# Performance work log

Measured on AMD Instinct MI355X. Metric: run time of the kernel, lower is better.

The kernel has to match this reference:

```python
import jax, jax.numpy as jnp
import numpy as np

MARGIN = 0.3
EPS = 1e-6  # torch pairwise_distance default eps used by TripletMarginLoss


def setup_inputs() -> dict:
    key = jax.random.key(0)
    k1, k2 = jax.random.split(key)
    emb = jax.random.normal(k1, (4096, 256), dtype=jnp.float32)
    emb = emb / jnp.linalg.norm(emb, axis=1, keepdims=True)  # docstring: normalized embeddings
    labels = jax.random.randint(k2, (4096,), 0, 64, dtype=jnp.int64) if jax.config.jax_enable_x64 else jax.random.randint(k2, (4096,), 0, 64, dtype=jnp.int32)
    return {"embeddings": emb, "labels": labels}


def _triplet_mining_loss(embeddings, labels):
    B = embeddings.shape[0]
    # pairwise euclidean distances via GEMM (matches torch.cdist p=2)
    sq = jnp.sum(embeddings * embeddings, axis=1)
    d2 = sq[:, None] + sq[None, :] - 2.0 * (embeddings @ embeddings.T)
    dist = jnp.sqrt(jnp.maximum(d2, 0.0))  # [B, B]

    same = labels[:, None] == labels[None, :]
    eye = jnp.eye(B, dtype=bool)
    pos_mask = same & ~eye
    neg_mask = ~same
    valid = pos_mask.any(axis=1) & neg_mask.any(axis=1)

    # hardest positive per anchor
    ap = jnp.where(pos_mask, dist, -jnp.inf)
    hp_idx = jnp.argmax(ap, axis=1)                           # [B]
    ap_dist = jnp.take_along_axis(dist, hp_idx[:, None], 1)[:, 0]

    # semi-hard negative: ap < d_an < ap + margin; pick FIRST such index (original takes semi_hard_indices[0])
    semi = neg_mask & (dist > ap_dist[:, None]) & (dist < ap_dist[:, None] + MARGIN)
    any_semi = semi.any(axis=1)
    first_semi = jnp.argmax(semi, axis=1)                     # argmax of bool = first True
    an = jnp.where(neg_mask, dist, jnp.inf)
    hardest_neg = jnp.argmin(an, axis=1)
    neg_idx = jnp.where(any_semi, first_semi, hardest_neg)

    # triplet margin loss recomputed from embeddings (torch adds EPS inside the norm)
    pos_e = embeddings[hp_idx]
    neg_e = embeddings[neg_idx]
    d_ap = jnp.linalg.norm(embeddings - pos_e + EPS, axis=1)
    d_an = jnp.linalg.norm(embeddings - neg_e + EPS, axis=1)
    per_anchor = jnp.maximum(d_ap - d_an + MARGIN, 0.0)

    vf = valid.astype(embeddings.dtype)
    cnt = jnp.sum(vf)
    return jnp.where(cnt > 0, jnp.sum(per_anchor * vf) / jnp.maximum(cnt, 1.0), 0.0)


def reference(embeddings, labels):
    return _triplet_mining_loss(embeddings, labels)
```

## Files before the change

### kernel.cpp

```cpp
#include <hip/hip_runtime.h>
#include <math.h>

#define BN 4096
#define DIM 256
#define D4 (DIM/4)
#define MI 8
#define MARGINF 0.3f
#define EPSF 1e-6f
#define SCAP 96
#define IMAX 0x7fffffff
#define PCAP 128

typedef __attribute__((ext_vector_type(8))) short bf16x8;
typedef __attribute__((ext_vector_type(4))) float f32x4;

__device__ __forceinline__ float fma4(float4 a, float4 b, float c){
  return fmaf(a.x,b.x, fmaf(a.y,b.y, fmaf(a.z,b.z, fmaf(a.w,b.w, c))));
}
__device__ __forceinline__ unsigned short f2bf(float x){
  unsigned u = __float_as_uint(x);
  return (unsigned short)((u + 0x7FFFu + ((u>>16)&1u)) >> 16);
}
__device__ __forceinline__ float bf2f(unsigned short h){
  return __uint_as_float(((unsigned)h)<<16);
}

__global__ __launch_bounds__(256) void k_pre2(const float* __restrict__ E,
     const int* __restrict__ labels,
     unsigned short* __restrict__ EhiT, unsigned short* __restrict__ EloT,
     float* __restrict__ sq, unsigned int* __restrict__ counter,
     unsigned short* __restrict__ memb, int* __restrict__ cntC,
     unsigned long long* __restrict__ negKey, unsigned int* __restrict__ semiJ){
  int t = threadIdx.x, l = t&63, w = t>>6;
  int g = blockIdx.x;
  const float4* E4 = (const float4*)E;
  bf16x8* HT = (bf16x8*)EhiT;
  bf16x8* LT = (bf16x8*)EloT;
  #pragma unroll
  for (int it=0; it<2; it++){
    int idx = it*256 + t;
    int kk = idx>>6, sub = idx&63, q = sub>>4, n = sub&15;
    int r = g*16 + n;
    int c = kk*4 + q;
    float4 v0 = E4[(size_t)r*64 + c*2];
    float4 v1 = E4[(size_t)r*64 + c*2 + 1];
    unsigned short h[8], lo[8];
    float vv[8] = {v0.x,v0.y,v0.z,v0.w, v1.x,v1.y,v1.z,v1.w};
    #pragma unroll
    for (int i=0;i<8;i++){ h[i]=f2bf(vv[i]); lo[i]=f2bf(vv[i]-bf2f(h[i])); }
    bf16x8 hv, lv;
    #pragma unroll
    for (int i=0;i<8;i++){ hv[i]=(short)h[i]; lv[i]=(short)lo[i]; }
    size_t d = (size_t)g*512 + idx;
    HT[d] = hv; LT[d] = lv;
  }
  int row = t>>4, part = t&15;
  const float4* rp = E4 + (size_t)(g*16+row)*64 + part*4;
  float s0 = fma4(rp[0],rp[0],0.f);
  float s1 = fma4(rp[1],rp[1],0.f);
  s0 = fma4(rp[2],rp[2],s0);
  s1 = fma4(rp[3],rp[3],s1);
  float s = s0+s1;
  s += __shfl_xor(s,1); s += __shfl_xor(s,2); s += __shfl_xor(s,4); s += __shfl_xor(s,8);
  if (part==0) sq[g*16+row] = s;
  if (g==0 && t==0) counter[0] = 0u;

  if (g < 16){
    int c = g*4 + w;
    int cnt = 0;
    for (int ch=0; ch<64; ch++){
      int j = ch*64 + l;
      bool m = (labels[j] == c);
      unsigned long long mask = __ballot(m);
      if (m){
        int pos = cnt + __popcll(mask & ((1ull<<l)-1ull));
        if (pos < PCAP-4) memb[c*PCAP + pos] = (unsigned short)j;
      }
      cnt += __popcll(mask);
    }
    if (cnt > PCAP-4) cnt = PCAP-4;
    if (l < 4) memb[c*PCAP + cnt + l] = 0;
    if (l == 0) cntC[c] = cnt;
  } else if (g < 32){
    int i = (g-16)*256 + t;
    negKey[i] = ~0ull;
    semiJ[i]  = 0xFFFFFFFFu;
  }
}

__global__ __launch_bounds__(256) void k_posm(const float* __restrict__ E,
     const int* __restrict__ labels, const float* __restrict__ sq,
     const unsigned short* __restrict__ memb, const int* __restrict__ cntC,
     float* __restrict__ apw, int* __restrict__ hpw){
  int t=threadIdx.x, l=t&63, w=t>>6;
  int aw = blockIdx.x*4 + w;
  int c = labels[aw];
  float sqa = sq[aw];
  const float4* E4 = (const float4*)E;
  float4 areg = E4[(size_t)aw*64 + l];
  int cnt = cntC[c];
  const unsigned short* lst = memb + c*PCAP;
  float bv2 = -INFINITY; int bj = IMAX;
  #pragma unroll 2
  for (int base=0; base<cnt; base+=4){
    int j0 = lst[base+0], j1 = lst[base+1], j2 = lst[base+2], j3 = lst[base+3];
    float4 r0v = E4[(size_t)j0*64 + l];
    float4 r1v = E4[(size_t)j1*64 + l];
    float4 r2v = E4[(size_t)j2*64 + l];
    float4 r3v = E4[(size_t)j3*64 + l];
    float p0 = fma4(areg, r0v, 0.f);
    float p1 = fma4(areg, r1v, 0.f);
    float p2 = fma4(areg, r2v, 0.f);
    float p3 = fma4(areg, r3v, 0.f);
    #pragma unroll
    for (int off=32; off; off>>=1){
      p0 += __shfl_xor(p0, off); p1 += __shfl_xor(p1, off);
      p2 += __shfl_xor(p2, off); p3 += __shfl_xor(p3, off);
    }
    float d0 = sqa + sq[j0] - 2.0f*p0;
    float d1 = sqa + sq[j1] - 2.0f*p1;
    float d2 = sqa + sq[j2] - 2.0f*p2;
    float d3 = sqa + sq[j3] - 2.0f*p3;
    if (j0 != aw && (d0 > bv2 || (d0 == bv2 && j0 < bj))){ bv2=d0; bj=j0; }
    if (base+1 < cnt && j1 != aw && (d1 > bv2 || (d1 == bv2 && j1 < bj))){ bv2=d1; bj=j1; }
    if (base+2 < cnt && j2 != aw && (d2 > bv2 || (d2 == bv2 && j2 < bj))){ bv2=d2; bj=j2; }
    if (base+3 < cnt && j3 != aw && (d3 > bv2 || (d3 == bv2 && j3 < bj))){ bv2=d3; bj=j3; }
  }
  if (l==0){
    apw[aw] = (bj==IMAX) ? -INFINITY : sqrtf(fmaxf(bv2, 0.0f));
    hpw[aw] = (bj==IMAX) ? 0 : bj;
  }
}

__global__ __launch_bounds__(1024,4) void k_negm(
     const unsigned short* __restrict__ EhiT, const unsigned short* __restrict__ EloT,
     const int* __restrict__ labels, const float* __restrict__ sq,
     const float* __restrict__ apw,
     unsigned long long* __restrict__ negKey, unsigned int* __restrict__ semiJ){
  __shared__ bf16x8 afH[1024];
  __shared__ bf16x8 afL[1024];
  __shared__ __align__(16) int   labsH[1024];
  __shared__ __align__(16) float sqH[1024];
  __shared__ float rnv[16][32]; __shared__ int rnj[16][32]; __shared__ int rsm[16][32];
  int t=threadIdx.x, l=t&63, w=t>>6;
  int lane16 = l&15, quad = l>>4;
  int q8    = blockIdx.x & 7;
  int split = q8 >> 1;
  int grp   = (blockIdx.x >> 3)*2 + (q8 & 1);
  int a0 = grp*32;
  int hbase = split*1024;
  const bf16x8* HT = (const bf16x8*)EhiT;
  const bf16x8* LT = (const bf16x8*)EloT;
  afH[t] = HT[(size_t)grp*1024 + t];
  afL[t] = LT[(size_t)grp*1024 + t];
  labsH[t] = labels[hbase + t];
  sqH[t]   = sq[hbase + t];
  float sqa[2][4]; int laba[2][4]; float ap2[2][4]; float th2[2][4];
  #pragma unroll
  for (int g=0; g<2; g++){
    #pragma unroll
    for (int r=0; r<4; r++){
      int ag = a0 + g*16 + quad*4 + r;
      sqa[g][r] = sq[ag]; laba[g][r] = labels[ag];
      float ap = apw[ag];
      ap2[g][r] = ap*ap;
      float th = ap + MARGINF;
      th2[g][r] = th*th;
    }
  }
  __syncthreads();
  float mn[2][4]; int mj[2][4]; int sm[2][4];
  #pragma unroll
  for (int g=0; g<2; g++)
    #pragma unroll
    for (int r=0; r<4; r++){ mn[g][r]=INFINITY; mj[g][r]=IMAX; sm[g][r]=IMAX; }
  #pragma unroll 1
  for (int tile=0; tile<4; tile++){
    int gl = w*4 + tile;
    size_t BBase = (size_t)(split*64 + gl) * 512;
    f32x4 acc00={0.f,0.f,0.f,0.f}, acc01=acc00, acc02=acc00;
    f32x4 acc10=acc00, acc11=acc00, acc12=acc00;
    #pragma unroll 2
    for (int kk=0; kk<8; kk++){
      bf16x8 bh  = HT[BBase + kk*64 + l];
      bf16x8 bl  = LT[BBase + kk*64 + l];
      bf16x8 ah0 = afH[kk*64 + l];
      bf16x8 al0 = afL[kk*64 + l];
      bf16x8 ah1 = afH[512 + kk*64 + l];
      bf16x8 al1 = afL[512 + kk*64 + l];
      acc00 = __builtin_amdgcn_mfma_f32_16x16x32_bf16(ah0, bh, acc00, 0,0,0);
      acc01 = __builtin_amdgcn_mfma_f32_16x16x32_bf16(ah0, bl, acc01, 0,0,0);
      acc02 = __builtin_amdgcn_mfma_f32_16x16x32_bf16(al0, bh, acc02, 0,0,0);
      acc10 = __builtin_amdgcn_mfma_f32_16x16x32_bf16(ah1, bh, acc10, 0,0,0);
      acc11 = __builtin_amdgcn_mfma_f32_16x16x32_bf16(ah1, bl, acc11, 0,0,0);
      acc12 = __builtin_amdgcn_mfma_f32_16x16x32_bf16(al1, bh, acc12, 0,0,0);
    }
    int jloc = gl*16 + lane16;
    int lj = labsH[jloc]; float sqj = sqH[jloc];
    int jglob = hbase + jloc;
    #pragma unroll
    for (int r=0; r<4; r++){
      float dot0 = acc00[r] + (acc01[r] + acc02[r]);
      float d20  = sqa[0][r] + sqj - 2.0f*dot0;
      if (lj != laba[0][r]){
        if (d20 < mn[0][r]){ mn[0][r]=d20; mj[0][r]=jglob; }
        if (d20 > ap2[0][r] && d20 < th2[0][r] && jglob < sm[0][r]) sm[0][r]=jglob;
      }
      float dot1 = acc10[r] + (acc11[r] + acc12[r]);
      float d21  = sqa[1][r] + sqj - 2.0f*dot1;
      if (lj != laba[1][r]){
        if (d21 < mn[1][r]){ mn[1][r]=d21; mj[1][r]=jglob; }
        if (d21 > ap2[1][r] && d21 < th2[1][r] && jglob < sm[1][r]) sm[1][r]=jglob;
      }
    }
  }
  #pragma unroll
  for (int g=0; g<2; g++){
    #pragma unroll
    for (int r=0; r<4; r++){
      float v=mn[g][r]; int j=mj[g][r]; int s=sm[g][r];
      #pragma unroll
      for (int off=1; off<16; off<<=1){
        float v2=__shfl_xor(v,off); int j2=__shfl_xor(j,off); int s2=__shfl_xor(s,off);
        if (v2<v || (v2==v && j2<j)){ v=v2; j=j2; }
        s = (s2<s)?s2:s;
      }
      if (lane16==0){
        int ai = g*16 + quad*4 + r;
        rnv[w][ai]=v; rnj[w][ai]=j; rsm[w][ai]=s;
      }
    }
  }
  __syncthreads();
  if (t < 32){
    float V=INFINITY; int J=IMAX; int S=IMAX;
    for (int q=0; q<16; q++){
      float v2=rnv[q][t]; int j2=rnj[q][t];
      if (v2<V || (v2==V && j2<J)){ V=v2; J=j2; }
      int s2=rsm[q][t]; S=(s2<S)?s2:S;
    }
    unsigned u = __float_as_uint(V);
    unsigned key = (u & 0x80000000u) ? ~u : (u | 0x80000000u);
    unsigned long long k64 = (((unsigned long long)key)<<32) | (unsigned)J;
    atomicMin(&negKey[a0+t], k64);
    if (S != IMAX) atomicMin(&semiJ[a0+t], (unsigned)S);
  }
}

__global__ __launch_bounds__(256) void k_fin2(const float* __restrict__ E,
     const float* __restrict__ apw, const int* __restrict__ hpw,
     const unsigned long long* __restrict__ negKey, const unsigned int* __restrict__ semiJ,
     float* __restrict__ partials, unsigned int* __restrict__ counter,
     float* __restrict__ out){
  __shared__ float lsumS[4], lcntS[4];
  __shared__ float rs[4], rc[4];
  __shared__ int lastFlag;
  int t=threadIdx.x, l=t&63, w=t>>6;
  const float4* E4 = (const float4*)E;
  float lsum=0.f, lcnt=0.f;
  #pragma unroll 1
  for (int i=0;i<4;i++){
    int a = blockIdx.x*16 + w*4 + i;
    unsigned long long k64 = negKey[a];
    unsigned Jn = (unsigned)(k64 & 0xFFFFFFFFull);
    unsigned Sn = semiJ[a];
    bool anyneg = (Jn != (unsigned)IMAX);
    int ng = (Sn != 0xFFFFFFFFu) ? (int)Sn : (int)Jn;
    float ap = apw[a];
    bool dov = (ap != -INFINITY) && anyneg;
    if (dov){
      int hp = hpw[a];
      float4 av = E4[(size_t)a*64 + l];
      float4 pv = E4[(size_t)hp*64 + l];
      float4 nv = E4[(size_t)ng*64 + l];
      float d0=av.x-pv.x+EPSF, d1=av.y-pv.y+EPSF, d2=av.z-pv.z+EPSF, d3=av.w-pv.w+EPSF;
      float sp = fmaf(d0,d0, fmaf(d1,d1, fmaf(d2,d2, d3*d3)));
      float n0=av.x-nv.x+EPSF, n1=av.y-nv.y+EPSF, n2=av.z-nv.z+EPSF, n3=av.w-nv.w+EPSF;
      float sn = fmaf(n0,n0, fmaf(n1,n1, fmaf(n2,n2, n3*n3)));
      #pragma unroll
      for (int off=32; off; off>>=1){ sp += __shfl_xor(sp,off); sn += __shfl_xor(sn,off); }
      lsum += fmaxf(sqrtf(sp)-sqrtf(sn)+MARGINF, 0.0f);
      lcnt += 1.0f;
    }
  }
  if (l==0){ lsumS[w]=lsum; lcntS[w]=lcnt; }
  __syncthreads();
  if (t==0){
    partials[2*blockIdx.x]   = (lsumS[0]+lsumS[1])+(lsumS[2]+lsumS[3]);
    partials[2*blockIdx.x+1] = (lcntS[0]+lcntS[1])+(lcntS[2]+lcntS[3]);
    __threadfence();
    unsigned int old = atomicAdd(counter, 1u);
    lastFlag = (old == gridDim.x - 1) ? 1 : 0;
  }
  __syncthreads();
  if (lastFlag){
    __threadfence();
    float s = partials[2*t], c = partials[2*t+1];
    #pragma unroll
    for (int off=32; off; off>>=1){ s += __shfl_xor(s,off); c += __shfl_xor(c,off); }
    if (l==0){ rs[w]=s; rc[w]=c; }
    __syncthreads();
    if (t==0){
      float S=(rs[0]+rs[1])+(rs[2]+rs[3]);
      float C=(rc[0]+rc[1])+(rc[2]+rc[3]);
      out[0] = (C>0.0f) ? S/fmaxf(C,1.0f) : 0.0f;
    }
  }
}

__global__ __launch_bounds__(256) void k_sq(const float* __restrict__ E, float* __restrict__ sq){
  int i = blockIdx.x*256 + threadIdx.x;
  if (i >= BN) return;
  const float4* r = (const float4*)E + (size_t)i*D4;
  float a0=0.f,a1=0.f,a2=0.f,a3=0.f;
  #pragma unroll
  for (int q=0;q<D4;q+=4){
    a0 = fma4(r[q],r[q],a0);   a1 = fma4(r[q+1],r[q+1],a1);
    a2 = fma4(r[q+2],r[q+2],a2); a3 = fma4(r[q+3],r[q+3],a3);
  }
  sq[i] = (a0+a1)+(a2+a3);
}

__global__ __launch_bounds__(256) void k_pos(const float* __restrict__ E, const int* __restrict__ labels,
                       const float* __restrict__ sq, float* __restrict__ apw,
                       int* __restrict__ hpw, int* __restrict__ anypw){
  __shared__ int members[1024];
  __shared__ float4 mem4[SCAP*65];
  __shared__ int cnts[16][4];
  __shared__ int offs[16][4];
  __shared__ int cntS;
  int t = threadIdx.x, lane = t&63, w = t>>6;
  int c = blockIdx.x >> 2, split = blockIdx.x & 3;
  for (int ch=0; ch<16; ch++){
    bool m = (labels[ch*256 + t] == c);
    unsigned long long mask = __ballot(m);
    if (lane==0) cnts[ch][w] = __popcll(mask);
  }
  __syncthreads();
  if (t==0){
    int run=0;
    for (int ch=0; ch<16; ch++)
      for (int q=0;q<4;q++){ offs[ch][q]=run; run+=cnts[ch][q]; }
    cntS = run;
  }
  __syncthreads();
  int cnt = cntS; if (cnt>1024) cnt=1024;
  for (int ch=0; ch<16; ch++){
    int idx = ch*256 + t;
    bool m = (labels[idx] == c);
    unsigned long long mask = __ballot(m);
    int my = __popcll(mask & ((1ull<<lane)-1ull));
    int pos = offs[ch][w] + my;
    if (m && pos < 1024) members[pos] = idx;
  }
  int S = (cnt < SCAP) ? cnt : SCAP;
  int anyp = (cnt >= 2) ? 1 : 0;
  __syncthreads();
  const float4* E4 = (const float4*)E;
  for (int idx=t; idx<S*64; idx+=256){
    int row = idx>>6, f = idx&63;
    mem4[row*65 + f] = E4[(size_t)members[row]*D4 + f];
  }
  __syncthreads();
  int esplit = split*4 + w;
  int p = lane&3, cand = lane>>2;
  int passes = (cnt+15)>>4;
  for (int mi=esplit; mi<cnt; mi+=16){
    int i = members[mi];
    float sqi = sq[i];
    float4 ai4[16];
    if (mi < S){
      #pragma unroll
      for (int m=0;m<16;m++) ai4[m] = mem4[mi*65 + p + 4*m];
    } else {
      #pragma unroll
      for (int m=0;m<16;m++) ai4[m] = E4[(size_t)i*D4 + p + 4*m];
    }
    float bv = -INFINITY; int bj = IMAX;
    for (int ps=0; ps<passes; ps++){
      int mj = ps*16 + cand;
      if (mj < cnt && mj != mi){
        int j = members[mj];
        float a0v=0.f, a1v=0.f;
        if (mj < S){
          const float4* rj = mem4 + mj*65 + p;
          #pragma unroll
          for (int m=0;m<16;m+=2){ a0v=fma4(ai4[m],rj[4*m],a0v); a1v=fma4(ai4[m+1],rj[4*(m+1)],a1v); }
        } else {
          const float4* rj = E4 + (size_t)j*D4 + p;
          #pragma unroll
          for (int m=0;m<16;m+=2){ a0v=fma4(ai4[m],rj[4*m],a0v); a1v=fma4(ai4[m+1],rj[4*(m+1)],a1v); }
        }
        float acc = a0v+a1v;
        acc += __shfl_xor(acc,1); acc += __shfl_xor(acc,2);
        float d = sqrtf(fmaxf(sqi + sq[j] - 2.0f*acc, 0.0f));
        if (p==0){ if (d > bv || (d==bv && j<bj)){ bv=d; bj=j; } }
      }
    }
    #pragma unroll
    for (int off=32; off; off>>=1){
      float v2=__shfl_xor(bv,off); int j2=__shfl_xor(bj,off);
      if (v2>bv || (v2==bv && j2<bj)){ bv=v2; bj=j2; }
    }
    if (lane==0){
      int J = (bj==IMAX) ? 0 : bj;
      apw[i]=bv; hpw[i]=J; anypw[i]=anyp;
    }
  }
}

__global__ __launch_bounds__(256,2) void k_main(const float* __restrict__ E, const int* __restrict__ labels,
     const float* __restrict__ sq, const float* __restrict__ apw, const int* __restrict__ hpw,
     const int* __restrict__ anypw, float* __restrict__ partials){
  __shared__ float4 At[MI*68 + 4];
  __shared__ float redv[4][MI]; __shared__ int redj[4][MI]; __shared__ int redsm[4][MI];
  __shared__ int finNeg[MI]; __shared__ int finVal[MI];
  __shared__ float redp[4], redn[4];
  int t=threadIdx.x, lane=t&63, w=t>>6;
  int a0 = blockIdx.x * MI;
  const float4* E4 = (const float4*)E;
  for (int idx=t; idx<MI*64; idx+=256){
    int a=idx>>6, q=idx&63, pp=q&3, mm=q>>2;
    At[a*68 + pp*17 + mm] = E4[(size_t)(a0+a)*D4 + q];
  }
  __syncthreads();
  float apv[MI], sqi[MI]; int labi[MI];
  #pragma unroll
  for (int a=0;a<MI;a++){ apv[a]=apw[a0+a]; sqi[a]=sq[a0+a]; labi[a]=labels[a0+a]; }
  float mnv[MI]; int mnj[MI]; int smj[MI];
  #pragma unroll
  for (int a=0;a<MI;a++){ mnv[a]=INFINITY; mnj[a]=0; smj[a]=IMAX; }
  int s = t>>2, p = t&3;
  for (int it=0; it<16; it++){
    int colb = it*256 + 4*s;
    const float4* __restrict__ bp = E4 + (size_t)colb*D4 + p;
    float acc[MI][4];
    #pragma unroll
    for (int a=0;a<MI;a++){
      #pragma unroll
      for (int c2=0;c2<4;c2++) acc[a][c2]=0.0f;
    }
    for (int mg=0; mg<4; mg++){
      float4 b[4][4];
      #pragma unroll
      for (int c2=0;c2<4;c2++){
        #pragma unroll
        for (int m=0;m<4;m++) b[m][c2] = bp[(size_t)c2*D4 + mg*16 + m*4];
      }
      #pragma unroll
      for (int a=0;a<MI;a++){
        float4 a4[4];
        #pragma unroll
        for (int m=0;m<4;m++) a4[m] = At[a*68 + p*17 + mg*4 + m];
        #pragma unroll
        for (int m=0;m<4;m++){
          #pragma unroll
          for (int c2=0;c2<4;c2++) acc[a][c2] = fma4(a4[m], b[m][c2], acc[a][c2]);
        }
      }
    }
    #pragma unroll
    for (int a=0;a<MI;a++){
      #pragma unroll
      for (int c2=0;c2<4;c2++){
        float v = acc[a][c2];
        v += __shfl_xor(v,1); v += __shfl_xor(v,2);
        acc[a][c2] = v;
      }
    }
    #pragma unroll
    for (int c2=0;c2<4;c2++){
      int j = colb + c2;
      int lj = labels[j]; float sqj = sq[j];
      #pragma unroll
      for (int a=0;a<MI;a++){
        float d = sqrtf(fmaxf(sqi[a]+sqj-2.0f*acc[a][c2], 0.0f));
        if (lj != labi[a]){
          if (d < mnv[a]){ mnv[a]=d; mnj[a]=j; }
          if (d > apv[a] && d < apv[a]+MARGINF && j < smj[a]) smj[a]=j;
        }
      }
    }
  }
  #pragma unroll
  for (int a=0;a<MI;a++){
    float v=mnv[a]; int j=mnj[a]; int sm=smj[a];
    #pragma unroll
    for (int off=32; off; off>>=1){
      float v2=__shfl_xor(v,off); int j2=__shfl_xor(j,off); int s2=__shfl_xor(sm,off);
      if (v2<v || (v2==v && j2<j)){ v=v2; j=j2; }
      sm = (s2<sm)?s2:sm;
    }
    if (lane==0){ redv[w][a]=v; redj[w][a]=j; redsm[w][a]=sm; }
  }
  __syncthreads();
  if (t < MI){
    int a=t;
    float V=INFINITY; int J=0; int S=IMAX; bool first=true;
    for (int q=0;q<4;q++){
      float v2=redv[q][a]; int j2=redj[q][a];
      if (first || v2<V || (v2==V && j2<J)){ V=v2; J=j2; first=false; }
      int s2=redsm[q][a]; S=(s2<S)?s2:S;
    }
    bool anyneg = (V < INFINITY);
    finNeg[a] = (S != IMAX) ? S : J;
    finVal[a] = (anypw[a0+a] != 0 && anyneg) ? 1 : 0;
  }
  __syncthreads();
  float lsum=0.0f, lcnt=0.0f;
  for (int a=0;a<MI;a++){
    if (finVal[a]){
      int hp = hpw[a0+a]; int ng = finNeg[a];
      float ai = E[(size_t)(a0+a)*DIM + t];
      float pv = E[(size_t)hp*DIM + t];
      float nv = E[(size_t)ng*DIM + t];
      float dp = ai - pv + EPSF; float dn = ai - nv + EPSF;
      float sp = dp*dp, sn = dn*dn;
      #pragma unroll
      for (int off=32; off; off>>=1){ sp += __shfl_xor(sp,off); sn += __shfl_xor(sn,off); }
      if (lane==0){ redp[w]=sp; redn[w]=sn; }
    }
    __syncthreads();
    if (finVal[a] && t==0){
      float SP=(redp[0]+redp[1])+(redp[2]+redp[3]);
      float SN=(redn[0]+redn[1])+(redn[2]+redn[3]);
      lsum += fmaxf(sqrtf(SP)-sqrtf(SN)+MARGINF, 0.0f);
      lcnt += 1.0f;
    }
    __syncthreads();
  }
  if (t==0){ partials[2*blockIdx.x]=lsum; partials[2*blockIdx.x+1]=lcnt; }
}

__global__ __launch_bounds__(256) void k_fin(const float* __restrict__ partials, float* __restrict__ out, int nb){
  __shared__ float rs[4], rc[4];
  int t=threadIdx.x, lane=t&63, w=t>>6;
  float s=0.f, c=0.f;
  for (int q=t;q<nb;q+=256){ s+=partials[2*q]; c+=partials[2*q+1]; }
  #pragma unroll
  for (int off=32; off; off>>=1){ s+=__shfl_xor(s,off); c+=__shfl_xor(c,off); }
  if (lane==0){ rs[w]=s; rc[w]=c; }
  __syncthreads();
  if (t==0){
    float S=(rs[0]+rs[1])+(rs[2]+rs[3]);
    float C=(rc[0]+rc[1])+(rc[2]+rc[3]);
    out[0] = (C>0.0f) ? S/fmaxf(C,1.0f) : 0.0f;
  }
}

extern "C" void kernel_launch(void* const* d_in, const int* in_sizes, int n_in,
                              void* d_out, int out_size, void* d_ws, size_t ws_size,
                              hipStream_t stream) {
  const float* E      = (const float*)d_in[0];
  const int*   labels = (const int*)d_in[1];
  float* out = (float*)d_out;

  float* sqw      = (float*)d_ws;
  float* apw      = sqw + BN;
  int*   hpw      = (int*)(apw + BN);
  int*   anypw    = hpw + BN;
  float* partials = (float*)(anypw + BN);
  unsigned int* counter = (unsigned int*)(partials + 1024);
  unsigned long long* negKey = (unsigned long long*)((char*)d_ws + 72*1024);
  unsigned int*       semiJ  = (unsigned int*)((char*)d_ws + 104*1024);
  unsigned short* memb = (unsigned short*)((char*)d_ws + 48*1024);
  int* cntC = (int*)((char*)d_ws + 120*1024);
  unsigned short* EhiT = (unsigned short*)((char*)d_ws + 131072);
  unsigned short* EloT = EhiT + (size_t)BN*DIM;
  bool big = ws_size >= (size_t)(131072 + 4*1024*1024);

  if (big){
    k_pre2<<<256,  256,  0, stream>>>(E, labels, EhiT, EloT, sqw, counter, memb, cntC, negKey, semiJ);
    k_posm<<<1024, 256,  0, stream>>>(E, labels, sqw, memb, cntC, apw, hpw);
    k_negm<<<512,  1024, 0, stream>>>(EhiT, EloT, labels, sqw, apw, negKey, semiJ);
    k_fin2<<<256,  256,  0, stream>>>(E, apw, hpw, negKey, semiJ, partials, counter, out);
  } else {
    k_sq  <<<BN/256, 256, 0, stream>>>(E, sqw);
    k_pos <<<256,    256, 0, stream>>>(E, labels, sqw, apw, hpw, anypw);
    k_main<<<BN/MI,  256, 0, stream>>>(E, labels, sqw, apw, hpw, anypw, partials);
    k_fin <<<1,      256, 0, stream>>>(partials, out, BN/MI);
  }
}
```

Baseline: 162.8 us.

## Fuse positive mining, negative mining and final loss into one kernel

Merges the hardest-positive kernel, the MFMA negative-mining kernel and the final loss kernel into one fused kernel. Each block now computes its own anchors' positives, then mines negatives over half of the candidates (2048 instead of 1024, with a 256-block grid). The last of the two blocks per anchor group finishes that group's loss and accumulates it through fixed-point 64-bit atomics, and a global done counter triggers the final division. The preprocessing kernel stages rows in LDS, parallelises the label-membership scan across waves and software-prefetches the B fragments. This cuts two launches and the global round trips, at the cost of halving the grid, which may lower occupancy and add serial positive-mining work per block.

```diff
diff --git a/kernel.cpp b/kernel.cpp
--- a/kernel.cpp
+++ b/kernel.cpp
@@ -10,6 +10,7 @@
 #define SCAP 96
 #define IMAX 0x7fffffff
 #define PCAP 128
+#define FXSCALE 1099511627776.0f
 
 typedef __attribute__((ext_vector_type(8))) short bf16x8;
 typedef __attribute__((ext_vector_type(4))) float f32x4;
@@ -25,176 +26,228 @@
   return __uint_as_float(((unsigned)h)<<16);
 }
 
-__global__ __launch_bounds__(256) void k_pre2(const float* __restrict__ E,
+__global__ __launch_bounds__(256) void k_pre(const float* __restrict__ E,
      const int* __restrict__ labels,
      unsigned short* __restrict__ EhiT, unsigned short* __restrict__ EloT,
-     float* __restrict__ sq, unsigned int* __restrict__ counter,
+     float* __restrict__ sq,
      unsigned short* __restrict__ memb, int* __restrict__ cntC,
-     unsigned long long* __restrict__ negKey, unsigned int* __restrict__ semiJ){
+     unsigned long long* __restrict__ negKey, unsigned int* __restrict__ semiJ,
+     int* __restrict__ cntA, unsigned long long* __restrict__ gsum,
+     unsigned long long* __restrict__ gcnt, unsigned int* __restrict__ done){
+  __shared__ float4 eS[16*65];
+  __shared__ unsigned long long msk[4][16];
+  __shared__ int wcnt[4];
   int t = threadIdx.x, l = t&63, w = t>>6;
   int g = blockIdx.x;
   const float4* E4 = (const float4*)E;
+  #pragma unroll
+  for (int it=0; it<4; it++){
+    int idx = it*256 + t;
+    int row = idx>>6, f = idx&63;
+    eS[row*65 + f] = E4[(size_t)g*1024 + idx];
+  }
+  __syncthreads();
   bf16x8* HT = (bf16x8*)EhiT;
   bf16x8* LT = (bf16x8*)EloT;
   #pragma unroll
   for (int it=0; it<2; it++){
-    int idx = it*256 + t;
-    int kk = idx>>6, sub = idx&63, q = sub>>4, n = sub&15;
-    int r = g*16 + n;
-    int c = kk*4 + q;
-    float4 v0 = E4[(size_t)r*64 + c*2];
-    float4 v1 = E4[(size_t)r*64 + c*2 + 1];
-    unsigned short h[8], lo[8];
+    int u = it*256 + t;
+    int kk = u>>6, sub = u&63, q = sub>>4, n = sub&15;
+    float4 v0 = eS[n*65 + kk*8 + q*2];
+    float4 v1 = eS[n*65 + kk*8 + q*2 + 1];
     float vv[8] = {v0.x,v0.y,v0.z,v0.w, v1.x,v1.y,v1.z,v1.w};
-    #pragma unroll
-    for (int i=0;i<8;i++){ h[i]=f2bf(vv[i]); lo[i]=f2bf(vv[i]-bf2f(h[i])); }
     bf16x8 hv, lv;
     #pragma unroll
-    for (int i=0;i<8;i++){ hv[i]=(short)h[i]; lv[i]=(short)lo[i]; }
-    size_t d = (size_t)g*512 + idx;
-    HT[d] = hv; LT[d] = lv;
-  }
-  int row = t>>4, part = t&15;
-  const float4* rp = E4 + (size_t)(g*16+row)*64 + part*4;
-  float s0 = fma4(rp[0],rp[0],0.f);
-  float s1 = fma4(rp[1],rp[1],0.f);
-  s0 = fma4(rp[2],rp[2],s0);
-  s1 = fma4(rp[3],rp[3],s1);
-  float s = s0+s1;
-  s += __shfl_xor(s,1); s += __shfl_xor(s,2); s += __shfl_xor(s,4); s += __shfl_xor(s,8);
-  if (part==0) sq[g*16+row] = s;
-  if (g==0 && t==0) counter[0] = 0u;
-
-  if (g < 16){
-    int c = g*4 + w;
-    int cnt = 0;
-    for (int ch=0; ch<64; ch++){
-      int j = ch*64 + l;
-      bool m = (labels[j] == c);
+    for (int i=0;i<8;i++){
+      unsigned short h = f2bf(vv[i]);
+      unsigned short lo = f2bf(vv[i]-bf2f(h));
+      hv[i]=(short)h; lv[i]=(short)lo;
+    }
+    HT[(size_t)g*512 + u] = hv;
+    LT[(size_t)g*512 + u] = lv;
+  }
+  {
+    int row = t>>4, part = t&15;
+    const float4* rp = &eS[row*65 + part*4];
+    float s0 = fma4(rp[0],rp[0],0.f);
+    float s1 = fma4(rp[1],rp[1],0.f);
+    s0 = fma4(rp[2],rp[2],s0);
+    s1 = fma4(rp[3],rp[3],s1);
+    float s = s0+s1;
+    s += __shfl_xor(s,1); s += __shfl_xor(s,2); s += __shfl_xor(s,4); s += __shfl_xor(s,8);
+    if (part==0) sq[g*16+row] = s;
+  }
+
+  if (g < 64){
+    int c = g;
+    int local = 0;
+    for (int i=0;i<16;i++){
+      int ch = w*16 + i;
+      bool m = (labels[ch*64 + l] == c);
       unsigned long long mask = __ballot(m);
+      if (l==0) msk[w][i] = mask;
+      local += __popcll(mask);
+    }
+    if (l==0) wcnt[w] = local;
+    __syncthreads();
+    int off = 0;
+    #pragma unroll
+    for (int q2=0; q2<4; q2++) if (q2 < w) off += wcnt[q2];
+    int total = wcnt[0]+wcnt[1]+wcnt[2]+wcnt[3];
+    int run = off;
+    for (int i=0;i<16;i++){
+      unsigned long long mask = msk[w][i];
+      int ch = w*16 + i;
+      bool m = (mask >> l) & 1ull;
       if (m){
-        int pos = cnt + __popcll(mask & ((1ull<<l)-1ull));
-        if (pos < PCAP-4) memb[c*PCAP + pos] = (unsigned short)j;
-      }
-      cnt += __popcll(mask);
-    }
-    if (cnt > PCAP-4) cnt = PCAP-4;
-    if (l < 4) memb[c*PCAP + cnt + l] = 0;
-    if (l == 0) cntC[c] = cnt;
-  } else if (g < 32){
-    int i = (g-16)*256 + t;
+        int pos = run + __popcll(mask & ((1ull<<l)-1ull));
+        if (pos < PCAP-4) memb[c*PCAP + pos] = (unsigned short)(ch*64 + l);
+      }
+      run += __popcll(mask);
+    }
+    if (total > PCAP-4) total = PCAP-4;
+    if (t < 4) memb[c*PCAP + total + t] = 0;
+    if (t == 0) cntC[c] = total;
+  } else if (g < 80){
+    int i = (g-64)*256 + t;
     negKey[i] = ~0ull;
     semiJ[i]  = 0xFFFFFFFFu;
-  }
-}
-
-__global__ __launch_bounds__(256) void k_posm(const float* __restrict__ E,
+  } else if (g == 80){
+    if (t < 128) cntA[t] = 0;
+    if (t == 128) *gsum = 0ull;
+    if (t == 129) *gcnt = 0ull;
+    if (t == 130) *done = 0u;
+  }
+}
+
+__global__ __launch_bounds__(1024,4) void k_fused(const float* __restrict__ E,
+     const unsigned short* __restrict__ EhiT, const unsigned short* __restrict__ EloT,
      const int* __restrict__ labels, const float* __restrict__ sq,
      const unsigned short* __restrict__ memb, const int* __restrict__ cntC,
-     float* __restrict__ apw, int* __restrict__ hpw){
-  int t=threadIdx.x, l=t&63, w=t>>6;
-  int aw = blockIdx.x*4 + w;
-  int c = labels[aw];
-  float sqa = sq[aw];
-  const float4* E4 = (const float4*)E;
-  float4 areg = E4[(size_t)aw*64 + l];
-  int cnt = cntC[c];
-  const unsigned short* lst = memb + c*PCAP;
-  float bv2 = -INFINITY; int bj = IMAX;
-  #pragma unroll 2
-  for (int base=0; base<cnt; base+=4){
-    int j0 = lst[base+0], j1 = lst[base+1], j2 = lst[base+2], j3 = lst[base+3];
-    float4 r0v = E4[(size_t)j0*64 + l];
-    float4 r1v = E4[(size_t)j1*64 + l];
-    float4 r2v = E4[(size_t)j2*64 + l];
-    float4 r3v = E4[(size_t)j3*64 + l];
-    float p0 = fma4(areg, r0v, 0.f);
-    float p1 = fma4(areg, r1v, 0.f);
-    float p2 = fma4(areg, r2v, 0.f);
-    float p3 = fma4(areg, r3v, 0.f);
-    #pragma unroll
-    for (int off=32; off; off>>=1){
-      p0 += __shfl_xor(p0, off); p1 += __shfl_xor(p1, off);
-      p2 += __shfl_xor(p2, off); p3 += __shfl_xor(p3, off);
-    }
-    float d0 = sqa + sq[j0] - 2.0f*p0;
-    float d1 = sqa + sq[j1] - 2.0f*p1;
-    float d2 = sqa + sq[j2] - 2.0f*p2;
-    float d3 = sqa + sq[j3] - 2.0f*p3;
-    if (j0 != aw && (d0 > bv2 || (d0 == bv2 && j0 < bj))){ bv2=d0; bj=j0; }
-    if (base+1 < cnt && j1 != aw && (d1 > bv2 || (d1 == bv2 && j1 < bj))){ bv2=d1; bj=j1; }
-    if (base+2 < cnt && j2 != aw && (d2 > bv2 || (d2 == bv2 && j2 < bj))){ bv2=d2; bj=j2; }
-    if (base+3 < cnt && j3 != aw && (d3 > bv2 || (d3 == bv2 && j3 < bj))){ bv2=d3; bj=j3; }
-  }
-  if (l==0){
-    apw[aw] = (bj==IMAX) ? -INFINITY : sqrtf(fmaxf(bv2, 0.0f));
-    hpw[aw] = (bj==IMAX) ? 0 : bj;
-  }
-}
-
-__global__ __launch_bounds__(1024,4) void k_negm(
-     const unsigned short* __restrict__ EhiT, const unsigned short* __restrict__ EloT,
-     const int* __restrict__ labels, const float* __restrict__ sq,
-     const float* __restrict__ apw,
-     unsigned long long* __restrict__ negKey, unsigned int* __restrict__ semiJ){
+     unsigned long long* __restrict__ negKey, unsigned int* __restrict__ semiJ,
+     int* __restrict__ cntA, unsigned long long* __restrict__ gsum,
+     unsigned long long* __restrict__ gcnt, unsigned int* __restrict__ done,
+     float* __restrict__ out){
   __shared__ bf16x8 afH[1024];
   __shared__ bf16x8 afL[1024];
-  __shared__ __align__(16) int   labsH[1024];
-  __shared__ __align__(16) float sqH[1024];
+  __shared__ __align__(16) int   labsH[2048];
+  __shared__ __align__(16) float sqH[2048];
   __shared__ float rnv[16][32]; __shared__ int rnj[16][32]; __shared__ int rsm[16][32];
+  __shared__ float apS[32]; __shared__ int hpS[32]; __shared__ int okS[32];
+  __shared__ float ap2S[32]; __shared__ float th2S[32];
+  __shared__ unsigned long long lfx; __shared__ unsigned int lcn;
+  __shared__ int lastFlag;
   int t=threadIdx.x, l=t&63, w=t>>6;
   int lane16 = l&15, quad = l>>4;
-  int q8    = blockIdx.x & 7;
-  int split = q8 >> 1;
-  int grp   = (blockIdx.x >> 3)*2 + (q8 & 1);
+  int q8   = blockIdx.x & 7;
+  int half = q8 >> 2;
+  int grp  = (blockIdx.x >> 3)*4 + (q8 & 3);
   int a0 = grp*32;
-  int hbase = split*1024;
+  int hbase = half*2048;
   const bf16x8* HT = (const bf16x8*)EhiT;
   const bf16x8* LT = (const bf16x8*)EloT;
+  const float4* E4 = (const float4*)E;
   afH[t] = HT[(size_t)grp*1024 + t];
   afL[t] = LT[(size_t)grp*1024 + t];
-  labsH[t] = labels[hbase + t];
-  sqH[t]   = sq[hbase + t];
+  { int2   lv = ((const int2*)(labels + hbase))[t];
+    labsH[2*t] = lv.x; labsH[2*t+1] = lv.y;
+    float2 sv = ((const float2*)(sq + hbase))[t];
+    sqH[2*t] = sv.x; sqH[2*t+1] = sv.y; }
+  if (t==0){ lfx = 0ull; lcn = 0u; }
+
+  for (int s=0; s<2; s++){
+    int ai = 2*w + s;
+    int aw = a0 + ai;
+    int c = labels[aw];
+    float sqa_ = sq[aw];
+    float4 areg = E4[(size_t)aw*64 + l];
+    int cn = cntC[c];
+    const unsigned short* lst = memb + c*PCAP;
+    float bv2 = -INFINITY; int bj = IMAX;
+    #pragma unroll 2
+    for (int base=0; base<cn; base+=4){
+      int j0 = lst[base+0], j1 = lst[base+1], j2 = lst[base+2], j3 = lst[base+3];
+      float4 r0v = E4[(size_t)j0*64 + l];
+      float4 r1v = E4[(size_t)j1*64 + l];
+      float4 r2v = E4[(size_t)j2*64 + l];
+      float4 r3v = E4[(size_t)j3*64 + l];
+      float p0 = fma4(areg, r0v, 0.f);
+      float p1 = fma4(areg, r1v, 0.f);
+      float p2 = fma4(areg, r2v, 0.f);
+      float p3 = fma4(areg, r3v, 0.f);
+      #pragma unroll
+      for (int off=32; off; off>>=1){
+        p0 += __shfl_xor(p0, off); p1 += __shfl_xor(p1, off);
+        p2 += __shfl_xor(p2, off); p3 += __shfl_xor(p3, off);
+      }
+      float d0 = sqa_ + sq[j0] - 2.0f*p0;
+      float d1 = sqa_ + sq[j1] - 2.0f*p1;
+      float d2 = sqa_ + sq[j2] - 2.0f*p2;
+      float d3 = sqa_ + sq[j3] - 2.0f*p3;
+      if (j0 != aw && (d0 > bv2 || (d0 == bv2 && j0 < bj))){ bv2=d0; bj=j0; }
+      if (base+1 < cn && j1 != aw && (d1 > bv2 || (d1 == bv2 && j1 < bj))){ bv2=d1; bj=j1; }
+      if (base+2 < cn && j2 != aw && (d2 > bv2 || (d2 == bv2 && j2 < bj))){ bv2=d2; bj=j2; }
+      if (base+3 < cn && j3 != aw && (d3 > bv2 || (d3 == bv2 && j3 < bj))){ bv2=d3; bj=j3; }
+    }
+    if (l==0){
+      okS[ai] = (bj != IMAX);
+      apS[ai] = (bj==IMAX) ? -INFINITY : sqrtf(fmaxf(bv2, 0.0f));
+      hpS[ai] = (bj==IMAX) ? 0 : bj;
+    }
+  }
+  __syncthreads();
+  if (t < 32){
+    float ap = apS[t];
+    ap2S[t] = ap*ap;
+    float th = ap + MARGINF;
+    th2S[t] = th*th;
+  }
+  __syncthreads();
+
   float sqa[2][4]; int laba[2][4]; float ap2[2][4]; float th2[2][4];
   #pragma unroll
   for (int g=0; g<2; g++){
     #pragma unroll
     for (int r=0; r<4; r++){
-      int ag = a0 + g*16 + quad*4 + r;
+      int ai = g*16 + quad*4 + r;
+      int ag = a0 + ai;
       sqa[g][r] = sq[ag]; laba[g][r] = labels[ag];
-      float ap = apw[ag];
-      ap2[g][r] = ap*ap;
-      float th = ap + MARGINF;
-      th2[g][r] = th*th;
-    }
-  }
-  __syncthreads();
+      ap2[g][r] = ap2S[ai]; th2[g][r] = th2S[ai];
+    }
+  }
+
   float mn[2][4]; int mj[2][4]; int sm[2][4];
   #pragma unroll
   for (int g=0; g<2; g++)
     #pragma unroll
     for (int r=0; r<4; r++){ mn[g][r]=INFINITY; mj[g][r]=IMAX; sm[g][r]=IMAX; }
+#define STEPK(KK,BH,BL) { \
+    bf16x8 ah0=afH[(KK)*64+l], al0=afL[(KK)*64+l]; \
+    bf16x8 ah1=afH[512+(KK)*64+l], al1=afL[512+(KK)*64+l]; \
+    acc00=__builtin_amdgcn_mfma_f32_16x16x32_bf16(ah0,BH,acc00,0,0,0); \
+    acc01=__builtin_amdgcn_mfma_f32_16x16x32_bf16(ah0,BL,acc01,0,0,0); \
+    acc02=__builtin_amdgcn_mfma_f32_16x16x32_bf16(al0,BH,acc02,0,0,0); \
+    acc10=__builtin_amdgcn_mfma_f32_16x16x32_bf16(ah1,BH,acc10,0,0,0); \
+    acc11=__builtin_amdgcn_mfma_f32_16x16x32_bf16(ah1,BL,acc11,0,0,0); \
+    acc12=__builtin_amdgcn_mfma_f32_16x16x32_bf16(al1,BH,acc12,0,0,0); }
   #pragma unroll 1
-  for (int tile=0; tile<4; tile++){
-    int gl = w*4 + tile;
-    size_t BBase = (size_t)(split*64 + gl) * 512;
+  for (int tile=0; tile<8; tile++){
+    int gl = w*8 + tile;
+    size_t BBase = (size_t)(half*128 + gl) * 512;
     f32x4 acc00={0.f,0.f,0.f,0.f}, acc01=acc00, acc02=acc00;
     f32x4 acc10=acc00, acc11=acc00, acc12=acc00;
-    #pragma unroll 2
-    for (int kk=0; kk<8; kk++){
-      bf16x8 bh  = HT[BBase + kk*64 + l];
-      bf16x8 bl  = LT[BBase + kk*64 + l];
-      bf16x8 ah0 = afH[kk*64 + l];
-      bf16x8 al0 = afL[kk*64 + l];
-      bf16x8 ah1 = afH[512 + kk*64 + l];
-      bf16x8 al1 = afL[512 + kk*64 + l];
-      acc00 = __builtin_amdgcn_mfma_f32_16x16x32_bf16(ah0, bh, acc00, 0,0,0);
-      acc01 = __builtin_amdgcn_mfma_f32_16x16x32_bf16(ah0, bl, acc01, 0,0,0);
-      acc02 = __builtin_amdgcn_mfma_f32_16x16x32_bf16(al0, bh, acc02, 0,0,0);
-      acc10 = __builtin_amdgcn_mfma_f32_16x16x32_bf16(ah1, bh, acc10, 0,0,0);
-      acc11 = __builtin_amdgcn_mfma_f32_16x16x32_bf16(ah1, bl, acc11, 0,0,0);
-      acc12 = __builtin_amdgcn_mfma_f32_16x16x32_bf16(al1, bh, acc12, 0,0,0);
-    }
+    bf16x8 bh0 = HT[BBase + 0*64 + l], bl0 = LT[BBase + 0*64 + l];
+    bf16x8 bh1 = HT[BBase + 1*64 + l], bl1 = LT[BBase + 1*64 + l];
+    bf16x8 bh2 = HT[BBase + 2*64 + l], bl2 = LT[BBase + 2*64 + l];
+    bf16x8 bh3 = HT[BBase + 3*64 + l], bl3 = LT[BBase + 3*64 + l];
+    STEPK(0,bh0,bl0); bh0 = HT[BBase + 4*64 + l]; bl0 = LT[BBase + 4*64 + l];
+    STEPK(1,bh1,bl1); bh1 = HT[BBase + 5*64 + l]; bl1 = LT[BBase + 5*64 + l];
+    STEPK(2,bh2,bl2); bh2 = HT[BBase + 6*64 + l]; bl2 = LT[BBase + 6*64 + l];
+    STEPK(3,bh3,bl3); bh3 = HT[BBase + 7*64 + l]; bl3 = LT[BBase + 7*64 + l];
+    STEPK(4,bh0,bl0);
+    STEPK(5,bh1,bl1);
+    STEPK(6,bh2,bl2);
+    STEPK(7,bh3,bl3);
     int jloc = gl*16 + lane16;
     int lj = labsH[jloc]; float sqj = sqH[jloc];
     int jglob = hbase + jloc;
@@ -214,6 +267,7 @@
       }
     }
   }
+#undef STEPK
   #pragma unroll
   for (int g=0; g<2; g++){
     #pragma unroll
@@ -245,65 +299,57 @@
     atomicMin(&negKey[a0+t], k64);
     if (S != IMAX) atomicMin(&semiJ[a0+t], (unsigned)S);
   }
-}
-
-__global__ __launch_bounds__(256) void k_fin2(const float* __restrict__ E,
-     const float* __restrict__ apw, const int* __restrict__ hpw,
-     const unsigned long long* __restrict__ negKey, const unsigned int* __restrict__ semiJ,
-     float* __restrict__ partials, unsigned int* __restrict__ counter,
-     float* __restrict__ out){
-  __shared__ float lsumS[4], lcntS[4];
-  __shared__ float rs[4], rc[4];
-  __shared__ int lastFlag;
-  int t=threadIdx.x, l=t&63, w=t>>6;
-  const float4* E4 = (const float4*)E;
-  float lsum=0.f, lcnt=0.f;
-  #pragma unroll 1
-  for (int i=0;i<4;i++){
-    int a = blockIdx.x*16 + w*4 + i;
-    unsigned long long k64 = negKey[a];
-    unsigned Jn = (unsigned)(k64 & 0xFFFFFFFFull);
-    unsigned Sn = semiJ[a];
-    bool anyneg = (Jn != (unsigned)IMAX);
-    int ng = (Sn != 0xFFFFFFFFu) ? (int)Sn : (int)Jn;
-    float ap = apw[a];
-    bool dov = (ap != -INFINITY) && anyneg;
-    if (dov){
-      int hp = hpw[a];
-      float4 av = E4[(size_t)a*64 + l];
-      float4 pv = E4[(size_t)hp*64 + l];
-      float4 nv = E4[(size_t)ng*64 + l];
-      float d0=av.x-pv.x+EPSF, d1=av.y-pv.y+EPSF, d2=av.z-pv.z+EPSF, d3=av.w-pv.w+EPSF;
-      float sp = fmaf(d0,d0, fmaf(d1,d1, fmaf(d2,d2, d3*d3)));
-      float n0=av.x-nv.x+EPSF, n1=av.y-nv.y+EPSF, n2=av.z-nv.z+EPSF, n3=av.w-nv.w+EPSF;
-      float sn = fmaf(n0,n0, fmaf(n1,n1, fmaf(n2,n2, n3*n3)));
-      #pragma unroll
-      for (int off=32; off; off>>=1){ sp += __shfl_xor(sp,off); sn += __shfl_xor(sn,off); }
-      lsum += fmaxf(sqrtf(sp)-sqrtf(sn)+MARGINF, 0.0f);
-      lcnt += 1.0f;
-    }
-  }
-  if (l==0){ lsumS[w]=lsum; lcntS[w]=lcnt; }
   __syncthreads();
   if (t==0){
-    partials[2*blockIdx.x]   = (lsumS[0]+lsumS[1])+(lsumS[2]+lsumS[3]);
-    partials[2*blockIdx.x+1] = (lcntS[0]+lcntS[1])+(lcntS[2]+lcntS[3]);
     __threadfence();
-    unsigned int old = atomicAdd(counter, 1u);
-    lastFlag = (old == gridDim.x - 1) ? 1 : 0;
+    int old = atomicAdd(&cntA[grp], 1);
+    lastFlag = (old == 1) ? 1 : 0;
   }
   __syncthreads();
   if (lastFlag){
     __threadfence();
-    float s = partials[2*t], c = partials[2*t+1];
-    #pragma unroll
-    for (int off=32; off; off>>=1){ s += __shfl_xor(s,off); c += __shfl_xor(c,off); }
-    if (l==0){ rs[w]=s; rc[w]=c; }
+    for (int s=0; s<2; s++){
+      int ai = 2*w + s;
+      int a = a0 + ai;
+      unsigned long long k64 = negKey[a];
+      unsigned Jn = (unsigned)(k64 & 0xFFFFFFFFull);
+      unsigned Sn = semiJ[a];
+      bool anyneg = (k64 != ~0ull);
+      int ng = (Sn != 0xFFFFFFFFu) ? (int)Sn : (int)Jn;
+      bool dov = (okS[ai] != 0) && anyneg;
+      float sp = 0.f, sn_ = 0.f;
+      if (dov){
+        int hp = hpS[ai];
+        float4 av = E4[(size_t)a*64 + l];
+        float4 pv = E4[(size_t)hp*64 + l];
+        float4 nv = E4[(size_t)ng*64 + l];
+        float d0=av.x-pv.x+EPSF, d1=av.y-pv.y+EPSF, d2=av.z-pv.z+EPSF, d3=av.w-pv.w+EPSF;
+        sp = fmaf(d0,d0, fmaf(d1,d1, fmaf(d2,d2, d3*d3)));
+        float n0=av.x-nv.x+EPSF, n1=av.y-nv.y+EPSF, n2=av.z-nv.z+EPSF, n3=av.w-nv.w+EPSF;
+        sn_ = fmaf(n0,n0, fmaf(n1,n1, fmaf(n2,n2, n3*n3)));
+      }
+      #pragma unroll
+      for (int off=32; off; off>>=1){ sp += __shfl_xor(sp,off); sn_ += __shfl_xor(sn_,off); }
+      if (l==0 && dov){
+        float loss = fmaxf(sqrtf(sp)-sqrtf(sn_)+MARGINF, 0.0f);
+        unsigned long long fx = (unsigned long long)llrintf(loss * FXSCALE);
+        atomicAdd(&lfx, fx);
+        atomicAdd(&lcn, 1u);
+      }
+    }
     __syncthreads();
     if (t==0){
-      float S=(rs[0]+rs[1])+(rs[2]+rs[3]);
-      float C=(rc[0]+rc[1])+(rc[2]+rc[3]);
-      out[0] = (C>0.0f) ? S/fmaxf(C,1.0f) : 0.0f;
+      atomicAdd(gsum, lfx);
+      atomicAdd(gcnt, (unsigned long long)lcn);
+      __threadfence();
+      unsigned int d = atomicAdd(done, 1u);
+      if (d == 127u){
+        __threadfence();
+        unsigned long long S = atomicAdd(gsum, 0ull);
+        unsigned long long C = atomicAdd(gcnt, 0ull);
+        double Sf = (double)S / 1099511627776.0;
+        out[0] = (C > 0ull) ? (float)(Sf / (double)C) : 0.0f;
+      }
     }
   }
 }
@@ -560,20 +606,23 @@
   int*   hpw      = (int*)(apw + BN);
   int*   anypw    = hpw + BN;
   float* partials = (float*)(anypw + BN);
-  unsigned int* counter = (unsigned int*)(partials + 1024);
   unsigned long long* negKey = (unsigned long long*)((char*)d_ws + 72*1024);
   unsigned int*       semiJ  = (unsigned int*)((char*)d_ws + 104*1024);
   unsigned short* memb = (unsigned short*)((char*)d_ws + 48*1024);
   int* cntC = (int*)((char*)d_ws + 120*1024);
+  int* cntA = (int*)((char*)d_ws + 121*1024);
+  unsigned long long* gsum = (unsigned long long*)((char*)d_ws + 122*1024);
+  unsigned long long* gcnt = gsum + 1;
+  unsigned int* done = (unsigned int*)(gsum + 2);
   unsigned short* EhiT = (unsigned short*)((char*)d_ws + 131072);
   unsigned short* EloT = EhiT + (size_t)BN*DIM;
   bool big = ws_size >= (size_t)(131072 + 4*1024*1024);
 
   if (big){
-    k_pre2<<<256,  256,  0, stream>>>(E, labels, EhiT, EloT, sqw, counter, memb, cntC, negKey, semiJ);
-    k_posm<<<1024, 256,  0, stream>>>(E, labels, sqw, memb, cntC, apw, hpw);
-    k_negm<<<512,  1024, 0, stream>>>(EhiT, EloT, labels, sqw, apw, negKey, semiJ);
-    k_fin2<<<256,  256,  0, stream>>>(E, apw, hpw, negKey, semiJ, partials, counter, out);
+    k_pre  <<<256, 256,  0, stream>>>(E, labels, EhiT, EloT, sqw, memb, cntC,
+                                      negKey, semiJ, cntA, gsum, gcnt, done);
+    k_fused<<<256, 1024, 0, stream>>>(E, EhiT, EloT, labels, sqw, memb, cntC,
+                                      negKey, semiJ, cntA, gsum, gcnt, done, out);
   } else {
     k_sq  <<<BN/256, 256, 0, stream>>>(E, sqw);
     k_pos <<<256,    256, 0, stream>>>(E, labels, sqw, apw, hpw, anypw);
```

Measured after the change: 378.5 us. 2.32x slower.

## Halve k_negm grid by splitting columns in two and software-prefetch B fragments

Applied to the files above, without the earlier changes.

Each k_negm block now covers half of the 4096 candidate columns (2048) instead of a quarter, so each wave processes 8 column tiles and the grid drops from 512 to 256 blocks. This halves the number of partial results per anchor and the redundant loads of the anchor fragments into shared memory. The k-loop is fully unrolled with a four-deep register prefetch of B fragments, meant to hide global-load latency behind MFMA work. Launch bounds are relaxed to one block per CU, which frees registers but reduces occupancy, and 256 blocks may underfill the GPU's CUs.

```diff
diff --git a/kernel.cpp b/kernel.cpp
--- a/kernel.cpp
+++ b/kernel.cpp
@@ -132,29 +132,31 @@
   }
 }
 
-__global__ __launch_bounds__(1024,4) void k_negm(
+__global__ __launch_bounds__(1024,1) void k_negm(
      const unsigned short* __restrict__ EhiT, const unsigned short* __restrict__ EloT,
      const int* __restrict__ labels, const float* __restrict__ sq,
      const float* __restrict__ apw,
      unsigned long long* __restrict__ negKey, unsigned int* __restrict__ semiJ){
   __shared__ bf16x8 afH[1024];
   __shared__ bf16x8 afL[1024];
-  __shared__ __align__(16) int   labsH[1024];
-  __shared__ __align__(16) float sqH[1024];
+  __shared__ __align__(16) int   labsH[2048];
+  __shared__ __align__(16) float sqH[2048];
   __shared__ float rnv[16][32]; __shared__ int rnj[16][32]; __shared__ int rsm[16][32];
   int t=threadIdx.x, l=t&63, w=t>>6;
   int lane16 = l&15, quad = l>>4;
-  int q8    = blockIdx.x & 7;
-  int split = q8 >> 1;
-  int grp   = (blockIdx.x >> 3)*2 + (q8 & 1);
+  int q8   = blockIdx.x & 7;
+  int half = q8 >> 2;
+  int grp  = (blockIdx.x >> 3)*4 + (q8 & 3);
   int a0 = grp*32;
-  int hbase = split*1024;
+  int hbase = half*2048;
   const bf16x8* HT = (const bf16x8*)EhiT;
   const bf16x8* LT = (const bf16x8*)EloT;
   afH[t] = HT[(size_t)grp*1024 + t];
   afL[t] = LT[(size_t)grp*1024 + t];
-  labsH[t] = labels[hbase + t];
-  sqH[t]   = sq[hbase + t];
+  { int2   lv = ((const int2*)(labels + hbase))[t];
+    labsH[2*t] = lv.x; labsH[2*t+1] = lv.y;
+    float2 sv = ((const float2*)(sq + hbase))[t];
+    sqH[2*t] = sv.x; sqH[2*t+1] = sv.y; }
   float sqa[2][4]; int laba[2][4]; float ap2[2][4]; float th2[2][4];
   #pragma unroll
   for (int g=0; g<2; g++){
@@ -174,27 +176,33 @@
   for (int g=0; g<2; g++)
     #pragma unroll
     for (int r=0; r<4; r++){ mn[g][r]=INFINITY; mj[g][r]=IMAX; sm[g][r]=IMAX; }
+#define STEPK(KK,BH,BL) { \
+    bf16x8 ah0=afH[(KK)*64+l], al0=afL[(KK)*64+l]; \
+    bf16x8 ah1=afH[512+(KK)*64+l], al1=afL[512+(KK)*64+l]; \
+    acc00=__builtin_amdgcn_mfma_f32_16x16x32_bf16(ah0,BH,acc00,0,0,0); \
+    acc01=__builtin_amdgcn_mfma_f32_16x16x32_bf16(ah0,BL,acc01,0,0,0); \
+    acc02=__builtin_amdgcn_mfma_f32_16x16x32_bf16(al0,BH,acc02,0,0,0); \
+    acc10=__builtin_amdgcn_mfma_f32_16x16x32_bf16(ah1,BH,acc10,0,0,0); \
+    acc11=__builtin_amdgcn_mfma_f32_16x16x32_bf16(ah1,BL,acc11,0,0,0); \
+    acc12=__builtin_amdgcn_mfma_f32_16x16x32_bf16(al1,BH,acc12,0,0,0); }
   #pragma unroll 1
-  for (int tile=0; tile<4; tile++){
-    int gl = w*4 + tile;
-    size_t BBase = (size_t)(split*64 + gl) * 512;
+  for (int tile=0; tile<8; tile++){
+    int gl = w*8 + tile;
+    size_t BBase = (size_t)(half*128 + gl) * 512;
     f32x4 acc00={0.f,0.f,0.f,0.f}, acc01=acc00, acc02=acc00;
     f32x4 acc10=acc00, acc11=acc00, acc12=acc00;
-    #pragma unroll 2
-    for (int kk=0; kk<8; kk++){
-      bf16x8 bh  = HT[BBase + kk*64 + l];
-      bf16x8 bl  = LT[BBase + kk*64 + l];
-      bf16x8 ah0 = afH[kk*64 + l];
-      bf16x8 al0 = afL[kk*64 + l];
-      bf16x8 ah1 = afH[512 + kk*64 + l];
-      bf16x8 al1 = afL[512 + kk*64 + l];
-      acc00 = __builtin_amdgcn_mfma_f32_16x16x32_bf16(ah0, bh, acc00, 0,0,0);
-      acc01 = __builtin_amdgcn_mfma_f32_16x16x32_bf16(ah0, bl, acc01, 0,0,0);
-      acc02 = __builtin_amdgcn_mfma_f32_16x16x32_bf16(al0, bh, acc02, 0,0,0);
-      acc10 = __builtin_amdgcn_mfma_f32_16x16x32_bf16(ah1, bh, acc10, 0,0,0);
-      acc11 = __builtin_amdgcn_mfma_f32_16x16x32_bf16(ah1, bl, acc11, 0,0,0);
-      acc12 = __builtin_amdgcn_mfma_f32_16x16x32_bf16(al1, bh, acc12, 0,0,0);
-    }
+    bf16x8 bh0 = HT[BBase + 0*64 + l], bl0 = LT[BBase + 0*64 + l];
+    bf16x8 bh1 = HT[BBase + 1*64 + l], bl1 = LT[BBase + 1*64 + l];
+    bf16x8 bh2 = HT[BBase + 2*64 + l], bl2 = LT[BBase + 2*64 + l];
+    bf16x8 bh3 = HT[BBase + 3*64 + l], bl3 = LT[BBase + 3*64 + l];
+    STEPK(0,bh0,bl0); bh0 = HT[BBase + 4*64 + l]; bl0 = LT[BBase + 4*64 + l];
+    STEPK(1,bh1,bl1); bh1 = HT[BBase + 5*64 + l]; bl1 = LT[BBase + 5*64 + l];
+    STEPK(2,bh2,bl2); bh2 = HT[BBase + 6*64 + l]; bl2 = LT[BBase + 6*64 + l];
+    STEPK(3,bh3,bl3); bh3 = HT[BBase + 7*64 + l]; bl3 = LT[BBase + 7*64 + l];
+    STEPK(4,bh0,bl0);
+    STEPK(5,bh1,bl1);
+    STEPK(6,bh2,bl2);
+    STEPK(7,bh3,bl3);
     int jloc = gl*16 + lane16;
     int lj = labsH[jloc]; float sqj = sqH[jloc];
     int jglob = hbase + jloc;
@@ -214,6 +222,7 @@
       }
     }
   }
+#undef STEPK
   #pragma unroll
   for (int g=0; g<2; g++){
     #pragma unroll
@@ -572,7 +581,7 @@
   if (big){
     k_pre2<<<256,  256,  0, stream>>>(E, labels, EhiT, EloT, sqw, counter, memb, cntC, negKey, semiJ);
     k_posm<<<1024, 256,  0, stream>>>(E, labels, sqw, memb, cntC, apw, hpw);
-    k_negm<<<512,  1024, 0, stream>>>(EhiT, EloT, labels, sqw, apw, negKey, semiJ);
+    k_negm<<<256,  1024, 0, stream>>>(EhiT, EloT, labels, sqw, apw, negKey, semiJ);
     k_fin2<<<256,  256,  0, stream>>>(E, apw, hpw, negKey, semiJ, partials, counter, out);
   } else {
     k_sq  <<<BN/256, 256, 0, stream>>>(E, sqw);
```

Measured after the change: 339.1 us. 108% more time.
